# Kernel tuning notes

Hardware: AMD Instinct MI355X
Metric: run time of the kernel (lower is better)

Reference implementation:

```python
import jax, jax.numpy as jnp
import numpy as np

ALPHA = 1.0 / 50.0  # dt / tau with dt=1, tau=50

T, B, I, H = 1024, 64, 128, 512


def setup_inputs() -> dict:
    key = jax.random.key(0)
    k1, k2, k3, k4 = jax.random.split(key, 4)
    x = jax.random.normal(k1, (T, B, I), dtype=jnp.float32)
    # input2h.weight ~ N(0, 0.5^2), shape [H, I]
    W_in = 0.5 * jax.random.normal(k2, (H, I), dtype=jnp.float32)
    # h2h.weight ~ N(0, 1/sqrt(H)^2), shape [H, H]
    W_h = jax.random.normal(k3, (H, H), dtype=jnp.float32) / np.sqrt(H).astype(np.float32)
    # initial_hidden ~ U(-1, 1), shape [1, H]
    h0 = jax.random.uniform(k4, (1, H), dtype=jnp.float32) * 2.0 - 1.0
    return {"x": x, "W_in": W_in, "W_h": W_h, "h0": h0}


def reference(x, W_in, W_h, h0):
    # Precompute input projection for all timesteps in one big GEMM:
    # [T, B, I] @ [I, H] -> [T, B, H]
    x_proj = jnp.einsum('tbi,hi->tbh', x, W_in)
    hidden0 = jnp.broadcast_to(h0, (x.shape[1], h0.shape[1]))  # [B, H]

    def step(hidden, xp_t):
        h_new = jax.nn.sigmoid(xp_t + hidden @ W_h.T)
        h_new = hidden * (1.0 - ALPHA) + h_new * ALPHA
        return h_new, h_new

    hidden_final, output = jax.lax.scan(step, hidden0, x_proj)
    return output, hidden_final
```

## Files before the change

kernel.cpp:

```cpp
#include <hip/hip_runtime.h>

#define T_STEPS 1024
#define BATCH   64
#define IDIM    128
#define HDIM    512
#define ALPHA_F 0.02f
#define NLOG2E  (-1.4426950408889634f)

typedef _Float16 half2_t __attribute__((ext_vector_type(2)));
typedef unsigned int uint32;

__device__ __forceinline__ float dot2f(uint32 w, uint32 h, float acc) {
#if __has_builtin(__builtin_amdgcn_fdot2)
  return __builtin_amdgcn_fdot2(__builtin_bit_cast(half2_t, w),
                                __builtin_bit_cast(half2_t, h), acc, false);
#else
  half2_t a = __builtin_bit_cast(half2_t, w);
  half2_t b = __builtin_bit_cast(half2_t, h);
  return acc + (float)a.x * (float)b.x + (float)a.y * (float)b.y;
#endif
}

__device__ __forceinline__ uint32 pk2(float a, float b) {
  auto p = __builtin_amdgcn_cvt_pkrtz(a, b);
  return __builtin_bit_cast(uint32, p);
}

__device__ __forceinline__ int dot4i8(uint32 a, uint32 b, int c) {
#if __has_builtin(__builtin_amdgcn_sdot4)
  return __builtin_amdgcn_sdot4((int)a, (int)b, c, false);
#else
  int s = c;
  s += (int)(signed char)(a)        * (int)(signed char)(b);
  s += (int)(signed char)(a >> 8)   * (int)(signed char)(b >> 8);
  s += (int)(signed char)(a >> 16)  * (int)(signed char)(b >> 16);
  s += (int)(signed char)(a >> 24)  * (int)(signed char)(b >> 24);
  return s;
#endif
}

__device__ __forceinline__ uint32 pkq(float v0, float v1, float v2, float v3, float inv) {
  int i0 = __float2int_rn(v0 * inv), i1 = __float2int_rn(v1 * inv);
  int i2 = __float2int_rn(v2 * inv), i3 = __float2int_rn(v3 * inv);
  return (uint32)(i0 & 255) | ((uint32)(i1 & 255) << 8) |
         ((uint32)(i2 & 255) << 16) | ((uint32)(i3 & 255) << 24);
}

__device__ __forceinline__ float fast_rcp(float x) {
#if __has_builtin(__builtin_amdgcn_rcpf)
  return __builtin_amdgcn_rcpf(x);
#else
  return 1.0f / x;
#endif
}

__device__ __forceinline__ int dpp_xor1(int x) {
#if __has_builtin(__builtin_amdgcn_mov_dpp)
  return __builtin_amdgcn_mov_dpp(x, 0xB1, 0xF, 0xF, true);
#else
  return __shfl_xor(x, 1);
#endif
}
__device__ __forceinline__ int dpp_xor2(int x) {
#if __has_builtin(__builtin_amdgcn_mov_dpp)
  return __builtin_amdgcn_mov_dpp(x, 0x4E, 0xF, 0xF, true);
#else
  return __shfl_xor(x, 2);
#endif
}
__device__ __forceinline__ int swz_xor4(int x) {
#if __has_builtin(__builtin_amdgcn_ds_swizzle)
  return __builtin_amdgcn_ds_swizzle(x, 0x101F);
#else
  return __shfl_xor(x, 4);
#endif
}
__device__ __forceinline__ float fxor1(float x) {
  return __builtin_bit_cast(float, dpp_xor1(__builtin_bit_cast(int, x)));
}
__device__ __forceinline__ float fxor2(float x) {
  return __builtin_bit_cast(float, dpp_xor2(__builtin_bit_cast(int, x)));
}
__device__ __forceinline__ float fxor4(float x) {
  return __builtin_bit_cast(float, swz_xor4(__builtin_bit_cast(int, x)));
}

__global__ __launch_bounds__(512) void ctrnn_proj(
    const float* __restrict__ x,
    const float* __restrict__ Win,
    float* __restrict__ xp,
    int rows) {
  const int j = threadIdx.x;
  __shared__ __attribute__((aligned(16))) uint32 xb[8][64];

  uint32 w[64];
  const float2* wr = (const float2*)(Win + (size_t)j * IDIM);
#pragma unroll
  for (int p = 0; p < 64; ++p) {
    float2 f = wr[p];
    w[p] = pk2(f.x, f.y);
  }

  const int m0 = blockIdx.x * 128;
  for (int it = 0; it < 16; ++it) {
    const int mb = m0 + it * 8;
    __syncthreads();
    if (j < 256) {
      const int r = j >> 5, q = j & 31;
      const int m = mb + r;
      float4 v = make_float4(0.f, 0.f, 0.f, 0.f);
      if (m < rows) v = *(const float4*)(x + (size_t)m * IDIM + q * 4);
      xb[r][2 * q]     = pk2(v.x, v.y);
      xb[r][2 * q + 1] = pk2(v.z, v.w);
    }
    __syncthreads();
#pragma unroll
    for (int r = 0; r < 8; ++r) {
      const int m = mb + r;
      if (m < rows) {
        const uint4* xv = (const uint4*)xb[r];
        float a0 = 0.f, a1 = 0.f, a2 = 0.f, a3 = 0.f;
#pragma unroll
        for (int c = 0; c < 16; ++c) {
          uint4 hx = xv[c];
          a0 = dot2f(w[4 * c + 0], hx.x, a0);
          a1 = dot2f(w[4 * c + 1], hx.y, a1);
          a2 = dot2f(w[4 * c + 2], hx.z, a2);
          a3 = dot2f(w[4 * c + 3], hx.w, a3);
        }
        xp[(size_t)m * HDIM + j] = NLOG2E * ((a0 + a1) + (a2 + a3));
      }
    }
  }
}

__global__ __launch_bounds__(512)
__attribute__((amdgpu_waves_per_eu(2, 2)))
void ctrnn_scan(
    const float* __restrict__ xp,
    const float* __restrict__ Wh,
    const float* __restrict__ h0,
    float* __restrict__ out,
    int t0, int ct) {
  const int b = blockIdx.x;
  const int j = threadIdx.x;
  const int g = j & 7;
  const int o = j >> 3;

  __shared__ __attribute__((aligned(16))) unsigned char hq[2][640];

  float m[8];
#pragma unroll
  for (int i = 0; i < 8; ++i) {
    const float4* wr = (const float4*)(Wh + (size_t)(8 * o + (i ^ g)) * HDIM + 64 * g);
    float mm = 0.f;
#pragma unroll
    for (int c = 0; c < 16; ++c) {
      float4 v = wr[c];
      mm = fmaxf(mm, fmaxf(fmaxf(fabsf(v.x), fabsf(v.y)), fmaxf(fabsf(v.z), fabsf(v.w))));
    }
    m[i] = mm;
  }
  {
    float t[8];
#pragma unroll
    for (int i = 0; i < 8; ++i) t[i] = fmaxf(m[i], fxor1(m[i ^ 1]));
#pragma unroll
    for (int i = 0; i < 8; ++i) m[i] = fmaxf(t[i], fxor2(t[i ^ 2]));
#pragma unroll
    for (int i = 0; i < 8; ++i) t[i] = fmaxf(m[i], fxor4(m[i ^ 4]));
#pragma unroll
    for (int i = 0; i < 8; ++i) m[i] = t[i];
  }

  uint32 w[128];
#pragma unroll
  for (int i = 0; i < 8; ++i) {
    const float rm = m[i];
    const float inv = (rm > 0.f) ? 127.f / rm : 0.f;
    const float4* wr = (const float4*)(Wh + (size_t)(8 * o + (i ^ g)) * HDIM + 64 * g);
#pragma unroll
    for (int c = 0; c < 16; ++c) {
      float4 v = wr[c];
      w[i * 16 + c] = pkq(v.x, v.y, v.z, v.w, inv);
    }
  }
  const float afac = m[0] * (1.f / (127.f * 127.f)) * NLOG2E;

  float h;
  if (t0 == 0) h = h0[j];
  else h = out[((size_t)(t0 - 1) * BATCH + b) * HDIM + j];
  hq[0][j + 16 * (j >> 6)] = (unsigned char)(__float2int_rn(h * 127.f));
  __syncthreads();

  const float* xpp = xp + (size_t)b * HDIM + j;
  float* outp = out + ((size_t)t0 * BATCH + b) * HDIM + j;
  const size_t BH = (size_t)BATCH * HDIM;

  int cur = 0;
#pragma unroll 2
  for (int t = 0; t < ct; ++t) {
    const float xpw = *xpp;

    const uint4* hb = (const uint4*)(&hq[cur][80 * g]);
    int a0 = 0, a1 = 0, a2 = 0, a3 = 0, a4 = 0, a5 = 0, a6 = 0, a7 = 0;
#pragma unroll
    for (int c = 0; c < 4; ++c) {
      const uint4 hv = hb[c];
      a0 = dot4i8(w[0 * 16 + 4 * c + 0], hv.x, a0);
      a0 = dot4i8(w[0 * 16 + 4 * c + 1], hv.y, a0);
      a0 = dot4i8(w[0 * 16 + 4 * c + 2], hv.z, a0);
      a0 = dot4i8(w[0 * 16 + 4 * c + 3], hv.w, a0);
      a1 = dot4i8(w[1 * 16 + 4 * c + 0], hv.x, a1);
      a1 = dot4i8(w[1 * 16 + 4 * c + 1], hv.y, a1);
      a1 = dot4i8(w[1 * 16 + 4 * c + 2], hv.z, a1);
      a1 = dot4i8(w[1 * 16 + 4 * c + 3], hv.w, a1);
      a2 = dot4i8(w[2 * 16 + 4 * c + 0], hv.x, a2);
      a2 = dot4i8(w[2 * 16 + 4 * c + 1], hv.y, a2);
      a2 = dot4i8(w[2 * 16 + 4 * c + 2], hv.z, a2);
      a2 = dot4i8(w[2 * 16 + 4 * c + 3], hv.w, a2);
      a3 = dot4i8(w[3 * 16 + 4 * c + 0], hv.x, a3);
      a3 = dot4i8(w[3 * 16 + 4 * c + 1], hv.y, a3);
      a3 = dot4i8(w[3 * 16 + 4 * c + 2], hv.z, a3);
      a3 = dot4i8(w[3 * 16 + 4 * c + 3], hv.w, a3);
      a4 = dot4i8(w[4 * 16 + 4 * c + 0], hv.x, a4);
      a4 = dot4i8(w[4 * 16 + 4 * c + 1], hv.y, a4);
      a4 = dot4i8(w[4 * 16 + 4 * c + 2], hv.z, a4);
      a4 = dot4i8(w[4 * 16 + 4 * c + 3], hv.w, a4);
      a5 = dot4i8(w[5 * 16 + 4 * c + 0], hv.x, a5);
      a5 = dot4i8(w[5 * 16 + 4 * c + 1], hv.y, a5);
      a5 = dot4i8(w[5 * 16 + 4 * c + 2], hv.z, a5);
      a5 = dot4i8(w[5 * 16 + 4 * c + 3], hv.w, a5);
      a6 = dot4i8(w[6 * 16 + 4 * c + 0], hv.x, a6);
      a6 = dot4i8(w[6 * 16 + 4 * c + 1], hv.y, a6);
      a6 = dot4i8(w[6 * 16 + 4 * c + 2], hv.z, a6);
      a6 = dot4i8(w[6 * 16 + 4 * c + 3], hv.w, a6);
      a7 = dot4i8(w[7 * 16 + 4 * c + 0], hv.x, a7);
      a7 = dot4i8(w[7 * 16 + 4 * c + 1], hv.y, a7);
      a7 = dot4i8(w[7 * 16 + 4 * c + 2], hv.z, a7);
      a7 = dot4i8(w[7 * 16 + 4 * c + 3], hv.w, a7);
    }
    const int q0 = a0 + dpp_xor1(a1);
    const int q1 = a2 + dpp_xor1(a3);
    const int q2 = a4 + dpp_xor1(a5);
    const int q3 = a6 + dpp_xor1(a7);
    const int r0 = q0 + dpp_xor2(q1);
    const int r1 = q2 + dpp_xor2(q3);
    const int res = r0 + swz_xor4(r1);

    const float e = exp2f((float)res * afac + xpw);
    const float s = fast_rcp(1.0f + e);
    h = h * (1.0f - ALPHA_F) + s * ALPHA_F;

    hq[cur ^ 1][j + 16 * (j >> 6)] = (unsigned char)(__float2int_rn(h * 127.f));
    __syncthreads();

    *outp = h;
    cur ^= 1;
    xpp += BH;
    outp += BH;
  }

  if (t0 + ct == T_STEPS) {
    out[(size_t)T_STEPS * BATCH * HDIM + (size_t)b * HDIM + j] = h;
  }
}

extern "C" void kernel_launch(void* const* d_in, const int* in_sizes, int n_in,
                              void* d_out, int out_size, void* d_ws, size_t ws_size,
                              hipStream_t stream) {
  const float* x   = (const float*)d_in[0];
  const float* Win = (const float*)d_in[1];
  const float* Wh  = (const float*)d_in[2];
  const float* h0  = (const float*)d_in[3];
  float* out = (float*)d_out;
  float* xp  = (float*)d_ws;

  const size_t step_bytes = (size_t)BATCH * HDIM * sizeof(float);
  int ct_max = (int)(ws_size / step_bytes);
  if (ct_max < 1) ct_max = 1;
  if (ct_max > T_STEPS) ct_max = T_STEPS;

  for (int t0 = 0; t0 < T_STEPS; t0 += ct_max) {
    const int ct = (T_STEPS - t0 < ct_max) ? (T_STEPS - t0) : ct_max;
    const int rows = ct * BATCH;
    const int nb = (rows + 127) / 128;
    hipLaunchKernelGGL(ctrnn_proj, dim3(nb), dim3(512), 0, stream,
                       x + (size_t)t0 * BATCH * IDIM, Win, xp, rows);
    hipLaunchKernelGGL(ctrnn_scan, dim3(BATCH), dim3(512), 0, stream,
                       xp, Wh, h0, out, t0, ct);
  }
}
```

Measured before the change: 884.7 us.

## Rewrite input projection kernel to use MFMA f16 matrix instructions

Replaces the dot2-based input projection GEMM with a kernel built on the 16x16x32 f16 MFMA instruction. Each wave holds a 16-column slice of W_in in registers and loops over 16-row tiles of x read straight from global memory, with no shared-memory staging. The goal is to shrink the projection phase ahead of the sequential scan, which probably dominates the total. The new kernel assumes rows is a multiple of 16 and drops the tail guard.

```diff
diff --git a/kernel.cpp b/kernel.cpp
--- a/kernel.cpp
+++ b/kernel.cpp
@@ -8,18 +8,9 @@
 #define NLOG2E  (-1.4426950408889634f)
 
 typedef _Float16 half2_t __attribute__((ext_vector_type(2)));
+typedef _Float16 f16x8 __attribute__((ext_vector_type(8)));
+typedef float f32x4 __attribute__((ext_vector_type(4)));
 typedef unsigned int uint32;
-
-__device__ __forceinline__ float dot2f(uint32 w, uint32 h, float acc) {
-#if __has_builtin(__builtin_amdgcn_fdot2)
-  return __builtin_amdgcn_fdot2(__builtin_bit_cast(half2_t, w),
-                                __builtin_bit_cast(half2_t, h), acc, false);
-#else
-  half2_t a = __builtin_bit_cast(half2_t, w);
-  half2_t b = __builtin_bit_cast(half2_t, h);
-  return acc + (float)a.x * (float)b.x + (float)a.y * (float)b.y;
-#endif
-}
 
 __device__ __forceinline__ uint32 pk2(float a, float b) {
   auto p = __builtin_amdgcn_cvt_pkrtz(a, b);
@@ -85,52 +76,47 @@
   return __builtin_bit_cast(float, swz_xor4(__builtin_bit_cast(int, x)));
 }
 
-__global__ __launch_bounds__(512) void ctrnn_proj(
+__device__ __forceinline__ f16x8 pk8(float4 lo, float4 hi) {
+  uint4 u = make_uint4(pk2(lo.x, lo.y), pk2(lo.z, lo.w),
+                       pk2(hi.x, hi.y), pk2(hi.z, hi.w));
+  return __builtin_bit_cast(f16x8, u);
+}
+
+__global__ __launch_bounds__(256) void ctrnn_proj_mfma(
     const float* __restrict__ x,
     const float* __restrict__ Win,
     float* __restrict__ xp,
     int rows) {
-  const int j = threadIdx.x;
-  __shared__ __attribute__((aligned(16))) uint32 xb[8][64];
-
-  uint32 w[64];
-  const float2* wr = (const float2*)(Win + (size_t)j * IDIM);
-#pragma unroll
-  for (int p = 0; p < 64; ++p) {
-    float2 f = wr[p];
-    w[p] = pk2(f.x, f.y);
-  }
-
-  const int m0 = blockIdx.x * 128;
-  for (int it = 0; it < 16; ++it) {
-    const int mb = m0 + it * 8;
-    __syncthreads();
-    if (j < 256) {
-      const int r = j >> 5, q = j & 31;
-      const int m = mb + r;
-      float4 v = make_float4(0.f, 0.f, 0.f, 0.f);
-      if (m < rows) v = *(const float4*)(x + (size_t)m * IDIM + q * 4);
-      xb[r][2 * q]     = pk2(v.x, v.y);
-      xb[r][2 * q + 1] = pk2(v.z, v.w);
-    }
-    __syncthreads();
-#pragma unroll
-    for (int r = 0; r < 8; ++r) {
-      const int m = mb + r;
-      if (m < rows) {
-        const uint4* xv = (const uint4*)xb[r];
-        float a0 = 0.f, a1 = 0.f, a2 = 0.f, a3 = 0.f;
-#pragma unroll
-        for (int c = 0; c < 16; ++c) {
-          uint4 hx = xv[c];
-          a0 = dot2f(w[4 * c + 0], hx.x, a0);
-          a1 = dot2f(w[4 * c + 1], hx.y, a1);
-          a2 = dot2f(w[4 * c + 2], hx.z, a2);
-          a3 = dot2f(w[4 * c + 3], hx.w, a3);
-        }
-        xp[(size_t)m * HDIM + j] = NLOG2E * ((a0 + a1) + (a2 + a3));
-      }
-    }
+  const int lane = threadIdx.x & 63;
+  const int wv   = threadIdx.x >> 6;
+  const int r16  = lane & 15;
+  const int kg   = lane >> 4;
+  const int jbase = (blockIdx.y * 4 + wv) * 16;
+
+  f16x8 bf[4];
+#pragma unroll
+  for (int kb = 0; kb < 4; ++kb) {
+    const float* wp = Win + (size_t)(jbase + r16) * IDIM + 32 * kb + 8 * kg;
+    float4 lo = *(const float4*)(wp);
+    float4 hi = *(const float4*)(wp + 4);
+    bf[kb] = pk8(lo, hi);
+  }
+
+  const int mtiles = rows >> 4;
+  for (int mt = blockIdx.x; mt < mtiles; mt += gridDim.x) {
+    const int mbase = mt << 4;
+    f32x4 acc = {0.f, 0.f, 0.f, 0.f};
+#pragma unroll
+    for (int kb = 0; kb < 4; ++kb) {
+      const float* xr = x + (size_t)(mbase + r16) * IDIM + 32 * kb + 8 * kg;
+      float4 lo = *(const float4*)(xr);
+      float4 hi = *(const float4*)(xr + 4);
+      acc = __builtin_amdgcn_mfma_f32_16x16x32_f16(pk8(lo, hi), bf[kb], acc, 0, 0, 0);
+    }
+    float* op = xp + (size_t)(mbase + 4 * kg) * HDIM + jbase + r16;
+#pragma unroll
+    for (int q = 0; q < 4; ++q)
+      op[(size_t)q * HDIM] = acc[q] * NLOG2E;
   }
 }
 
@@ -284,8 +270,9 @@
   for (int t0 = 0; t0 < T_STEPS; t0 += ct_max) {
     const int ct = (T_STEPS - t0 < ct_max) ? (T_STEPS - t0) : ct_max;
     const int rows = ct * BATCH;
-    const int nb = (rows + 127) / 128;
-    hipLaunchKernelGGL(ctrnn_proj, dim3(nb), dim3(512), 0, stream,
+    const int mtiles = rows >> 4;
+    const int gx = (mtiles < 256) ? mtiles : 256;
+    hipLaunchKernelGGL(ctrnn_proj_mfma, dim3(gx, 8), dim3(256), 0, stream,
                        x + (size_t)t0 * BATCH * IDIM, Win, xp, rows);
     hipLaunchKernelGGL(ctrnn_scan, dim3(BATCH), dim3(512), 0, stream,
                        xp, Wh, h0, out, t0, ct);
```

Measured after the change: 913.2 us. 3.2% more time.
